# Kernel tuning notes

Hardware: AMD Instinct MI355X
Metric: run time of the kernel (lower is better)

Reference implementation:

```python
import jax, jax.numpy as jnp
import numpy as np

EPS = 1e-5


def _bn(x, g, b, m, v):
    # eval-mode BatchNorm over the last (channel) axis
    return g * (x - m) * jax.lax.rsqrt(v + EPS) + b


def setup_inputs() -> dict:
    key = jax.random.key(0)
    ks = jax.random.split(key, 16)
    B, N, K, C, Cout, G = 2, 16384, 32, 64, 64, 10
    inp = {
        "points": jax.random.normal(ks[0], (B, N, 3), jnp.float32),
        "features": jax.random.normal(ks[1], (B, N, C), jnp.float32),
        "grouped_idx": jax.random.randint(ks[2], (B, N, K), 0, N, jnp.int32),
        # pos_proj: Conv2d(geo_ch, in_ch, 1) + BN + ReLU
        "W_pos": jax.random.normal(ks[3], (C, G), jnp.float32) / np.sqrt(G),
        "b_pos": jnp.zeros((C,), jnp.float32),
        "bn1_g": jnp.ones((C,), jnp.float32),
        "bn1_b": jnp.zeros((C,), jnp.float32),
        "bn1_m": jax.random.normal(ks[4], (C,), jnp.float32) * 0.1,
        "bn1_v": jax.random.uniform(ks[5], (C,), jnp.float32, 0.5, 1.5),
        # gcm_layer: Conv2d(in_ch, in_ch, 1) + BN + ReLU
        "W_gcm": jax.random.normal(ks[6], (C, C), jnp.float32) / np.sqrt(C),
        "b_gcm": jnp.zeros((C,), jnp.float32),
        "bn2_g": jnp.ones((C,), jnp.float32),
        "bn2_b": jnp.zeros((C,), jnp.float32),
        "bn2_m": jax.random.normal(ks[7], (C,), jnp.float32) * 0.1,
        "bn2_v": jax.random.uniform(ks[8], (C,), jnp.float32, 0.5, 1.5),
        # att_conv_catfea: Linear(nsample, 1)
        "W_att": jax.random.normal(ks[9], (K,), jnp.float32) / np.sqrt(K),
        "b_att": jnp.zeros((), jnp.float32),
        # out_layer: Linear(in_ch, out_ch) + LayerNorm + ReLU
        "W_out": jax.random.normal(ks[10], (Cout, C), jnp.float32) / np.sqrt(C),
        "b_out": jnp.zeros((Cout,), jnp.float32),
        "ln_g": jnp.ones((Cout,), jnp.float32),
        "ln_b": jnp.zeros((Cout,), jnp.float32),
    }
    return inp


def reference(points, features, grouped_idx, W_pos, b_pos, bn1_g, bn1_b, bn1_m, bn1_v,
              W_gcm, b_gcm, bn2_g, bn2_b, bn2_m, bn2_v, W_att, b_att,
              W_out, b_out, ln_g, ln_b):
    gather = jax.vmap(lambda arr, idx: arr[idx])  # [N,C],[N,K] -> [N,K,C]
    grouped_points = gather(points, grouped_idx)          # [B,N,K,3]
    grouped_f = gather(features, grouped_idx)             # [B,N,K,C]

    # legacy geometric encoding: [xi, xj, xi - xj, ||xi - xj||] -> geo_ch = 10
    xi = points[:, :, None, :]
    diff = xi - grouped_points
    dist = jnp.linalg.norm(diff, axis=-1, keepdims=True)
    geo = jnp.concatenate(
        [jnp.broadcast_to(xi, grouped_points.shape), grouped_points, diff, dist], axis=-1)

    # pos_proj: 1x1 conv == channel linear, + BN + ReLU
    expanded = jax.nn.relu(_bn(jnp.einsum('bnkg,cg->bnkc', geo, W_pos) + b_pos,
                               bn1_g, bn1_b, bn1_m, bn1_v))

    h = grouped_f + expanded
    # gcm_layer
    h = jax.nn.relu(_bn(jnp.einsum('bnkc,dc->bnkd', h, W_gcm) + b_gcm,
                        bn2_g, bn2_b, bn2_m, bn2_v))

    # attention over neighbor dim K -> score per channel, softmax over channels (dim=2 of [B,N,C,1])
    score = jnp.einsum('bnkc,k->bnc', h, W_att) + b_att   # [B,N,C]
    score = jax.nn.softmax(score, axis=-1)
    h = h * score[:, :, None, :]                          # [B,N,K,C]

    pooled = jnp.max(h, axis=2)                           # maxpooling downsample -> [B,N,C]
    res = pooled + features

    # out_layer: Linear + LayerNorm + ReLU
    y = jnp.einsum('bnc,oc->bno', res, W_out) + b_out
    mu = jnp.mean(y, axis=-1, keepdims=True)
    var = jnp.var(y, axis=-1, keepdims=True)
    y = ln_g * (y - mu) * jax.lax.rsqrt(var + EPS) + ln_b
    return jax.nn.relu(y)
```

## Files before the change

### kernel.cpp

```cpp
#include <hip/hip_runtime.h>
#include <hip/hip_bf16.h>

#define EPSF 1e-5f

typedef __attribute__((ext_vector_type(8))) short bf16x8;
typedef __attribute__((ext_vector_type(4))) float f32x4;
typedef __attribute__((ext_vector_type(2))) unsigned int u32x2;
typedef __attribute__((ext_vector_type(4))) unsigned int u32x4;
typedef __attribute__((ext_vector_type(4))) int i32x4;

constexpr int B_ = 2, N_ = 16384;
constexpr int HSTR = 72;
constexpr int RSTR = 72;
constexpr int PPW  = 8;
constexpr int NW   = 8;
constexpr int PPB  = 64;
constexpr int NWG  = (B_ * N_) / PPB;
constexpr int HALF = NWG / 2;
constexpr size_t PP_BYTES = (size_t)B_ * N_ * 16;

__device__ __forceinline__ short f2bf(float f) {
    __hip_bfloat16 h = __float2bfloat16(f);
    short s; __builtin_memcpy(&s, &h, 2); return s;
}
__device__ __forceinline__ unsigned int pkbf(float a, float b) {
    float2 f2; f2.x = a; f2.y = b;
    __hip_bfloat162 h = __float22bfloat162_rn(f2);
    unsigned int u; __builtin_memcpy(&u, &h, 4); return u;
}

__global__ __launch_bounds__(256) void prep_points(
    const float* __restrict__ pts, float* __restrict__ pp)
{
    const int i = blockIdx.x * 256 + threadIdx.x;
    if (i < B_ * N_) {
        f32x4 o = { pts[3 * i], pts[3 * i + 1], pts[3 * i + 2], 0.f };
        ((f32x4*)pp)[i] = o;
    }
}

template<bool PAD>
__global__ __launch_bounds__(512, 2) void bridgenet13(
    const float* __restrict__ points,
    const float* __restrict__ pp,
    const float* __restrict__ features,
    const int*   __restrict__ gidx,
    const float* __restrict__ Wpos,
    const float* __restrict__ bposv,
    const float* __restrict__ bn1g, const float* __restrict__ bn1b,
    const float* __restrict__ bn1m, const float* __restrict__ bn1v,
    const float* __restrict__ Wgcm,
    const float* __restrict__ bgcm,
    const float* __restrict__ bn2g, const float* __restrict__ bn2b,
    const float* __restrict__ bn2m, const float* __restrict__ bn2v,
    const float* __restrict__ Watt,
    const float* __restrict__ batt,
    const float* __restrict__ Wout,
    const float* __restrict__ bout,
    const float* __restrict__ lng, const float* __restrict__ lnb,
    float* __restrict__ out)
{
    __shared__ __align__(16) short hbuf[NW][32 * HSTR];
    __shared__ __align__(16) short resstage[PPB * RSTR];
    __shared__ __align__(16) short wb2[8 * 64 * 8];
    __shared__ __align__(16) short wb3[8 * 64 * 8];

    const int t    = threadIdx.x;
    const int w    = t >> 6;
    const int l    = t & 63;
    const int l15  = l & 15;
    const int quad = l >> 4;
    const int c4   = l15 * 4;

    const int wg  = blockIdx.x;
    const int blk = ((wg & 7) >> 2) * HALF + ((wg >> 3) << 2) + (wg & 3);

    {
        #pragma unroll
        for (int u = 0; u < 2; ++u) {
            const int s  = w * 2 + u;
            const int nt = (s >> 1) & 3, ks = s & 1;
            const float* src = (s < 8 ? Wgcm : Wout) + (c4 + nt) * 64 + ks * 32 + quad * 8;
            const f32x4 w0 = *(const f32x4*)src;
            const f32x4 w1 = *(const f32x4*)(src + 4);
            bf16x8 f;
            #pragma unroll
            for (int j = 0; j < 4; ++j) {
                f[j]     = f2bf(w0[j]);
                f[j + 4] = f2bf(w1[j]);
            }
            short* dst = (s < 8 ? wb2 : wb3);
            *(bf16x8*)&dst[((s & 7) * 64 + l) * 8] = f;
        }
    }

    bf16x8 bposf[4];
    #pragma unroll
    for (int nt = 0; nt < 4; ++nt) {
        const int c = c4 + nt;
        #pragma unroll
        for (int j = 0; j < 8; ++j) {
            const int g = quad * 8 + j;
            bposf[nt][j] = f2bf(g < 10 ? Wpos[c * 10 + g] : 0.f);
        }
    }
    f32x4 ps1, pb1, ps2, pb2;
    {
        const f32x4 g1 = *(const f32x4*)(bn1g + c4);
        const f32x4 b1 = *(const f32x4*)(bn1b + c4);
        const f32x4 m1 = *(const f32x4*)(bn1m + c4);
        const f32x4 v1 = *(const f32x4*)(bn1v + c4);
        const f32x4 bp = *(const f32x4*)(bposv + c4);
        const f32x4 g2 = *(const f32x4*)(bn2g + c4);
        const f32x4 b2 = *(const f32x4*)(bn2b + c4);
        const f32x4 m2 = *(const f32x4*)(bn2m + c4);
        const f32x4 v2 = *(const f32x4*)(bn2v + c4);
        const f32x4 bg = *(const f32x4*)(bgcm + c4);
        #pragma unroll
        for (int j = 0; j < 4; ++j) {
            ps1[j] = g1[j] * rsqrtf(v1[j] + EPSF);
            pb1[j] = ps1[j] * (bp[j] - m1[j]) + b1[j];
            ps2[j] = g2[j] * rsqrtf(v2[j] + EPSF);
            pb2[j] = ps2[j] * (bg[j] - m2[j]) + b2[j];
        }
    }
    float wat[2][4];
    #pragma unroll
    for (int mt = 0; mt < 2; ++mt)
        #pragma unroll
        for (int r = 0; r < 4; ++r)
            wat[mt][r] = Watt[mt * 16 + quad * 4 + r];
    const float battv = batt[0];

    const f32x4 zero4 = {0.f, 0.f, 0.f, 0.f};
    short* hb = hbuf[w];
    const int base = blk * PPB + w * PPW;
    const int bb   = ((blk * PPB) >> 14) * N_;

    const float* __restrict__ fb  = features + (size_t)bb * 64;
    const float* __restrict__ ppb = pp + (size_t)bb * 4;
    const int*   __restrict__ gb  = gidx + (size_t)base * 32;

    auto LOADI = [&](int i, i32x4 (&gi)[2]) {
        gi[0] = *(const i32x4*)(gb + i * 32 + quad * 4);
        gi[1] = *(const i32x4*)(gb + i * 32 + 16 + quad * 4);
    };
    auto LOADD = [&](int i, const i32x4 (&gi)[2],
                     f32x4 (&f4)[2][4], bf16x8 (&ageo)[2], f32x4& resid) {
        #pragma unroll
        for (int mt = 0; mt < 2; ++mt)
            #pragma unroll
            for (int r = 0; r < 4; ++r)
                f4[mt][r] = *(const f32x4*)(fb + (((unsigned)gi[mt][r]) << 6) + c4);
        const int pt = base + i;
        resid = *(const f32x4*)(features + (size_t)pt * 64 + c4);
        int gv[2];
        gv[0] = gb[i * 32 + l15];
        gv[1] = gb[i * 32 + 16 + l15];
        float xi0, xi1, xi2, px[2], py[2], pz[2];
        if (PAD) {
            const f32x4 x4 = *(const f32x4*)(pp + (size_t)pt * 4);
            xi0 = x4[0]; xi1 = x4[1]; xi2 = x4[2];
            #pragma unroll
            for (int mt = 0; mt < 2; ++mt) {
                const f32x4 p4 = *(const f32x4*)(ppb + (((unsigned)gv[mt]) << 2));
                px[mt] = p4[0]; py[mt] = p4[1]; pz[mt] = p4[2];
            }
        } else {
            xi0 = points[(size_t)pt * 3];
            xi1 = points[(size_t)pt * 3 + 1];
            xi2 = points[(size_t)pt * 3 + 2];
            #pragma unroll
            for (int mt = 0; mt < 2; ++mt) {
                const float* ppt = points + (size_t)(bb + gv[mt]) * 3;
                px[mt] = ppt[0]; py[mt] = ppt[1]; pz[mt] = ppt[2];
            }
        }
        #pragma unroll
        for (int mt = 0; mt < 2; ++mt) {
            const float dx = xi0 - px[mt], dy = xi1 - py[mt], dz = xi2 - pz[mt];
            const float dist = __builtin_amdgcn_sqrtf(dx * dx + dy * dy + dz * dz);
            u32x4 u = {0u, 0u, 0u, 0u};
            if (quad == 0) {
                u[0] = pkbf(xi0, xi1); u[1] = pkbf(xi2, px[mt]);
                u[2] = pkbf(py[mt], pz[mt]); u[3] = pkbf(dx, dy);
            } else if (quad == 1) {
                u[0] = pkbf(dz, dist);
            }
            __builtin_memcpy(&ageo[mt], &u, 16);
        }
    };

    auto COMPUTE = [&](const f32x4 (&f4)[2][4], const bf16x8 (&ageo)[2],
                       const f32x4& resid, int i) {
        __builtin_amdgcn_s_setprio(1);
        f32x4 acc1[2][4];
        #pragma unroll
        for (int mt = 0; mt < 2; ++mt)
            #pragma unroll
            for (int nt = 0; nt < 4; ++nt)
                acc1[mt][nt] = __builtin_amdgcn_mfma_f32_16x16x32_bf16(
                    ageo[mt], bposf[nt], zero4, 0, 0, 0);
        __builtin_amdgcn_s_setprio(0);

        #pragma unroll
        for (int mt = 0; mt < 2; ++mt)
            #pragma unroll
            for (int r = 0; r < 4; ++r) {
                const int k = mt * 16 + quad * 4 + r;
                float v[4];
                #pragma unroll
                for (int j = 0; j < 4; ++j)
                    v[j] = f4[mt][r][j] + fmaxf(ps1[j] * acc1[mt][j][r] + pb1[j], 0.f);
                u32x2 hv = { pkbf(v[0], v[1]), pkbf(v[2], v[3]) };
                *(u32x2*)&hb[k * HSTR + c4] = hv;
            }

        bf16x8 a2[2][2];
        #pragma unroll
        for (int mt = 0; mt < 2; ++mt)
            #pragma unroll
            for (int ks = 0; ks < 2; ++ks)
                a2[mt][ks] = *(const bf16x8*)&hb[(mt * 16 + l15) * HSTR + ks * 32 + quad * 8];
        __builtin_amdgcn_s_setprio(1);
        f32x4 acc2[2][4];
        #pragma unroll
        for (int nt = 0; nt < 4; ++nt) {
            const bf16x8 b0 = *(const bf16x8*)&wb2[((nt * 2 + 0) * 64 + l) * 8];
            const bf16x8 b1 = *(const bf16x8*)&wb2[((nt * 2 + 1) * 64 + l) * 8];
            #pragma unroll
            for (int mt = 0; mt < 2; ++mt) {
                f32x4 a = __builtin_amdgcn_mfma_f32_16x16x32_bf16(a2[mt][0], b0, zero4, 0, 0, 0);
                acc2[mt][nt] = __builtin_amdgcn_mfma_f32_16x16x32_bf16(a2[mt][1], b1, a, 0, 0, 0);
            }
        }
        __builtin_amdgcn_s_setprio(0);

        float res[4];
        {
            float sp[4], mk[4];
            #pragma unroll
            for (int nt = 0; nt < 4; ++nt) {
                sp[nt] = 0.f; mk[nt] = 0.f;
                #pragma unroll
                for (int mt = 0; mt < 2; ++mt)
                    #pragma unroll
                    for (int r = 0; r < 4; ++r) {
                        const float h2 = fmaxf(ps2[nt] * acc2[mt][nt][r] + pb2[nt], 0.f);
                        sp[nt] += h2 * wat[mt][r];
                        mk[nt] = fmaxf(mk[nt], h2);
                    }
                sp[nt] += __shfl_xor(sp[nt], 16);
                sp[nt] += __shfl_xor(sp[nt], 32);
                mk[nt] = fmaxf(mk[nt], __shfl_xor(mk[nt], 16));
                mk[nt] = fmaxf(mk[nt], __shfl_xor(mk[nt], 32));
            }
            float e[4], s = 0.f;
            #pragma unroll
            for (int nt = 0; nt < 4; ++nt) { e[nt] = __expf(sp[nt] + battv); s += e[nt]; }
            #pragma unroll
            for (int o = 1; o < 16; o <<= 1) s += __shfl_xor(s, o);
            const float inv = __builtin_amdgcn_rcpf(s);
            #pragma unroll
            for (int nt = 0; nt < 4; ++nt)
                res[nt] = e[nt] * inv * mk[nt] + resid[nt];
        }
        if (quad == 0) {
            u32x2 rv = { pkbf(res[0], res[1]), pkbf(res[2], res[3]) };
            *(u32x2*)&resstage[(w * PPW + i) * RSTR + c4] = rv;
        }
    };

    i32x4 giA[2], giB[2];
    LOADI(0, giA);
    LOADI(1, giB);
    f32x4  f4A[2][4], f4B[2][4];
    bf16x8 agA[2],   agB[2];
    f32x4  rsA,      rsB;
    LOADD(0, giA, f4A, agA, rsA);

    __syncthreads();

    for (int ip = 0; ip < PPW; ip += 2) {
        LOADD(ip + 1, giB, f4B, agB, rsB);
        if (ip + 2 < PPW) LOADI(ip + 2, giA);
        COMPUTE(f4A, agA, rsA, ip);
        if (ip + 2 < PPW) LOADD(ip + 2, giA, f4A, agA, rsA);
        if (ip + 3 < PPW) LOADI(ip + 3, giB);
        COMPUTE(f4B, agB, rsB, ip + 1);
    }

    __syncthreads();

    {
        const int g = w >> 1;
        const f32x4 lngv  = *(const f32x4*)(lng + c4);
        const f32x4 lnbv  = *(const f32x4*)(lnb + c4);
        const f32x4 boutv = *(const f32x4*)(bout + c4);
        bf16x8 a3[2];
        #pragma unroll
        for (int ks = 0; ks < 2; ++ks)
            a3[ks] = *(const bf16x8*)&resstage[(g * 16 + l15) * RSTR + ks * 32 + quad * 8];
        f32x4 acc3[4];
        #pragma unroll
        for (int nt = 0; nt < 4; ++nt) {
            const bf16x8 b0 = *(const bf16x8*)&wb3[((nt * 2 + 0) * 64 + l) * 8];
            const bf16x8 b1 = *(const bf16x8*)&wb3[((nt * 2 + 1) * 64 + l) * 8];
            f32x4 a = __builtin_amdgcn_mfma_f32_16x16x32_bf16(a3[0], b0, zero4, 0, 0, 0);
            acc3[nt] = __builtin_amdgcn_mfma_f32_16x16x32_bf16(a3[1], b1, a, 0, 0, 0);
        }
        #pragma unroll
        for (int u = 0; u < 2; ++u) {
            const int r = (w & 1) * 2 + u;
            float y[4], s = 0.f;
            #pragma unroll
            for (int nt = 0; nt < 4; ++nt) { y[nt] = acc3[nt][r] + boutv[nt]; s += y[nt]; }
            #pragma unroll
            for (int o = 1; o < 16; o <<= 1) s += __shfl_xor(s, o);
            const float mu = s * (1.f / 64.f);
            float dv[4], v2 = 0.f;
            #pragma unroll
            for (int nt = 0; nt < 4; ++nt) { dv[nt] = y[nt] - mu; v2 += dv[nt] * dv[nt]; }
            #pragma unroll
            for (int o = 1; o < 16; o <<= 1) v2 += __shfl_xor(v2, o);
            const float rs = rsqrtf(v2 * (1.f / 64.f) + EPSF);
            const int pto = blk * PPB + g * 16 + quad * 4 + r;
            f32x4 ov;
            #pragma unroll
            for (int nt = 0; nt < 4; ++nt)
                ov[nt] = fmaxf(lngv[nt] * dv[nt] * rs + lnbv[nt], 0.f);
            *(f32x4*)(out + (size_t)pto * 64 + c4) = ov;
        }
    }
}

extern "C" void kernel_launch(void* const* d_in, const int* in_sizes, int n_in,
                              void* d_out, int out_size, void* d_ws, size_t ws_size,
                              hipStream_t stream) {
    const float* points   = (const float*)d_in[0];
    const float* features = (const float*)d_in[1];
    const int*   gidxp    = (const int*)d_in[2];
    const bool   pad      = (ws_size >= PP_BYTES);
    float* pp = (float*)d_ws;
    if (pad) {
        hipLaunchKernelGGL(prep_points, dim3((B_ * N_ + 255) / 256), dim3(256), 0, stream,
                           points, pp);
        hipLaunchKernelGGL((bridgenet13<true>), dim3(NWG), dim3(512), 0, stream,
            points, pp, features, gidxp,
            (const float*)d_in[3],  (const float*)d_in[4],
            (const float*)d_in[5],  (const float*)d_in[6],  (const float*)d_in[7],  (const float*)d_in[8],
            (const float*)d_in[9],  (const float*)d_in[10],
            (const float*)d_in[11], (const float*)d_in[12], (const float*)d_in[13], (const float*)d_in[14],
            (const float*)d_in[15], (const float*)d_in[16],
            (const float*)d_in[17], (const float*)d_in[18],
            (const float*)d_in[19], (const float*)d_in[20],
            (float*)d_out);
    } else {
        hipLaunchKernelGGL((bridgenet13<false>), dim3(NWG), dim3(512), 0, stream,
            points, pp, features, gidxp,
            (const float*)d_in[3],  (const float*)d_in[4],
            (const float*)d_in[5],  (const float*)d_in[6],  (const float*)d_in[7],  (const float*)d_in[8],
            (const float*)d_in[9],  (const float*)d_in[10],
            (const float*)d_in[11], (const float*)d_in[12], (const float*)d_in[13], (const float*)d_in[14],
            (const float*)d_in[15], (const float*)d_in[16],
            (const float*)d_in[17], (const float*)d_in[18],
            (const float*)d_in[19], (const float*)d_in[20],
            (float*)d_out);
    }
}
```

Before: 157.4 us.

## Halve waves per block and interleave two points per wave with double-buffered LDS

Each block now runs 4 waves instead of 8, and each wave handles 16 points. The per-point compute is split into a FRONT stage (the two MFMA layers) and a BACK stage (attention, softmax, pooling). Two points are processed in parallel into separate LDS buffers, so the MFMA work of one point can hide the other's dependency chains, and gathers for the next pair are issued between stages. The cost is more registers per wave (four in-flight gather sets) and fewer waves per CU for hiding memory latency, with a risk of spills or lower occupancy.

```diff
diff --git a/kernel.cpp b/kernel.cpp
--- a/kernel.cpp
+++ b/kernel.cpp
@@ -12,8 +12,8 @@
 constexpr int B_ = 2, N_ = 16384;
 constexpr int HSTR = 72;
 constexpr int RSTR = 72;
-constexpr int PPW  = 8;
-constexpr int NW   = 8;
+constexpr int PPW  = 16;
+constexpr int NW   = 4;
 constexpr int PPB  = 64;
 constexpr int NWG  = (B_ * N_) / PPB;
 constexpr int HALF = NWG / 2;
@@ -40,7 +40,7 @@
 }
 
 template<bool PAD>
-__global__ __launch_bounds__(512, 2) void bridgenet13(
+__global__ __launch_bounds__(256, 2) void bridgenet14(
     const float* __restrict__ points,
     const float* __restrict__ pp,
     const float* __restrict__ features,
@@ -60,7 +60,7 @@
     const float* __restrict__ lng, const float* __restrict__ lnb,
     float* __restrict__ out)
 {
-    __shared__ __align__(16) short hbuf[NW][32 * HSTR];
+    __shared__ __align__(16) short hbuf[NW][2][32 * HSTR];
     __shared__ __align__(16) short resstage[PPB * RSTR];
     __shared__ __align__(16) short wb2[8 * 64 * 8];
     __shared__ __align__(16) short wb3[8 * 64 * 8];
@@ -77,8 +77,8 @@
 
     {
         #pragma unroll
-        for (int u = 0; u < 2; ++u) {
-            const int s  = w * 2 + u;
+        for (int u = 0; u < 4; ++u) {
+            const int s  = w * 4 + u;
             const int nt = (s >> 1) & 3, ks = s & 1;
             const float* src = (s < 8 ? Wgcm : Wout) + (c4 + nt) * 64 + ks * 32 + quad * 8;
             const f32x4 w0 = *(const f32x4*)src;
@@ -133,7 +133,6 @@
     const float battv = batt[0];
 
     const f32x4 zero4 = {0.f, 0.f, 0.f, 0.f};
-    short* hb = hbuf[w];
     const int base = blk * PPB + w * PPW;
     const int bb   = ((blk * PPB) >> 14) * N_;
 
@@ -191,8 +190,8 @@
         }
     };
 
-    auto COMPUTE = [&](const f32x4 (&f4)[2][4], const bf16x8 (&ageo)[2],
-                       const f32x4& resid, int i) {
+    auto FRONT = [&](short* hb, const f32x4 (&f4)[2][4], const bf16x8 (&ageo)[2],
+                     f32x4 (&acc2)[2][4]) {
         __builtin_amdgcn_s_setprio(1);
         f32x4 acc1[2][4];
         #pragma unroll
@@ -223,7 +222,6 @@
             for (int ks = 0; ks < 2; ++ks)
                 a2[mt][ks] = *(const bf16x8*)&hb[(mt * 16 + l15) * HSTR + ks * 32 + quad * 8];
         __builtin_amdgcn_s_setprio(1);
-        f32x4 acc2[2][4];
         #pragma unroll
         for (int nt = 0; nt < 4; ++nt) {
             const bf16x8 b0 = *(const bf16x8*)&wb2[((nt * 2 + 0) * 64 + l) * 8];
@@ -235,7 +233,9 @@
             }
         }
         __builtin_amdgcn_s_setprio(0);
-
+    };
+
+    auto BACK = [&](int i, const f32x4 (&acc2)[2][4], const f32x4& resid) {
         float res[4];
         {
             float sp[4], mk[4];
@@ -271,36 +271,57 @@
         }
     };
 
-    i32x4 giA[2], giB[2];
-    LOADI(0, giA);
-    LOADI(1, giB);
-    f32x4  f4A[2][4], f4B[2][4];
-    bf16x8 agA[2],   agB[2];
-    f32x4  rsA,      rsB;
-    LOADD(0, giA, f4A, agA, rsA);
+    short* hb0 = &hbuf[w][0][0];
+    short* hb1 = &hbuf[w][1][0];
+
+    i32x4 giA0[2], giA1[2], giB0[2], giB1[2];
+    LOADI(0, giA0); LOADI(1, giA1);
+    LOADI(2, giB0); LOADI(3, giB1);
+    f32x4  f4A0[2][4], f4A1[2][4], f4B0[2][4], f4B1[2][4];
+    bf16x8 agA0[2], agA1[2], agB0[2], agB1[2];
+    f32x4  rsA0, rsA1, rsB0, rsB1;
+    LOADD(0, giA0, f4A0, agA0, rsA0);
+    LOADD(1, giA1, f4A1, agA1, rsA1);
 
     __syncthreads();
 
-    for (int ip = 0; ip < PPW; ip += 2) {
-        LOADD(ip + 1, giB, f4B, agB, rsB);
-        if (ip + 2 < PPW) LOADI(ip + 2, giA);
-        COMPUTE(f4A, agA, rsA, ip);
-        if (ip + 2 < PPW) LOADD(ip + 2, giA, f4A, agA, rsA);
-        if (ip + 3 < PPW) LOADI(ip + 3, giB);
-        COMPUTE(f4B, agB, rsB, ip + 1);
+    #pragma unroll
+    for (int ip = 0; ip < PPW; ip += 4) {
+        f32x4 accA0[2][4], accA1[2][4];
+        FRONT(hb0, f4A0, agA0, accA0);
+        FRONT(hb1, f4A1, agA1, accA1);
+        if (ip + 2 < PPW) {
+            LOADD(ip + 2, giB0, f4B0, agB0, rsB0);
+            LOADD(ip + 3, giB1, f4B1, agB1, rsB1);
+            if (ip + 4 < PPW) { LOADI(ip + 4, giA0); LOADI(ip + 5, giA1); }
+        }
+        BACK(ip, accA0, rsA0);
+        BACK(ip + 1, accA1, rsA1);
+
+        if (ip + 2 < PPW) {
+            f32x4 accB0[2][4], accB1[2][4];
+            FRONT(hb0, f4B0, agB0, accB0);
+            FRONT(hb1, f4B1, agB1, accB1);
+            if (ip + 4 < PPW) {
+                LOADD(ip + 4, giA0, f4A0, agA0, rsA0);
+                LOADD(ip + 5, giA1, f4A1, agA1, rsA1);
+                if (ip + 6 < PPW) { LOADI(ip + 6, giB0); LOADI(ip + 7, giB1); }
+            }
+            BACK(ip + 2, accB0, rsB0);
+            BACK(ip + 3, accB1, rsB1);
+        }
     }
 
     __syncthreads();
 
     {
-        const int g = w >> 1;
         const f32x4 lngv  = *(const f32x4*)(lng + c4);
         const f32x4 lnbv  = *(const f32x4*)(lnb + c4);
         const f32x4 boutv = *(const f32x4*)(bout + c4);
         bf16x8 a3[2];
         #pragma unroll
         for (int ks = 0; ks < 2; ++ks)
-            a3[ks] = *(const bf16x8*)&resstage[(g * 16 + l15) * RSTR + ks * 32 + quad * 8];
+            a3[ks] = *(const bf16x8*)&resstage[(w * 16 + l15) * RSTR + ks * 32 + quad * 8];
         f32x4 acc3[4];
         #pragma unroll
         for (int nt = 0; nt < 4; ++nt) {
@@ -310,11 +331,10 @@
             acc3[nt] = __builtin_amdgcn_mfma_f32_16x16x32_bf16(a3[1], b1, a, 0, 0, 0);
         }
         #pragma unroll
-        for (int u = 0; u < 2; ++u) {
-            const int r = (w & 1) * 2 + u;
+        for (int u = 0; u < 4; ++u) {
             float y[4], s = 0.f;
             #pragma unroll
-            for (int nt = 0; nt < 4; ++nt) { y[nt] = acc3[nt][r] + boutv[nt]; s += y[nt]; }
+            for (int nt = 0; nt < 4; ++nt) { y[nt] = acc3[nt][u] + boutv[nt]; s += y[nt]; }
             #pragma unroll
             for (int o = 1; o < 16; o <<= 1) s += __shfl_xor(s, o);
             const float mu = s * (1.f / 64.f);
@@ -324,7 +344,7 @@
             #pragma unroll
             for (int o = 1; o < 16; o <<= 1) v2 += __shfl_xor(v2, o);
             const float rs = rsqrtf(v2 * (1.f / 64.f) + EPSF);
-            const int pto = blk * PPB + g * 16 + quad * 4 + r;
+            const int pto = blk * PPB + w * 16 + quad * 4 + u;
             f32x4 ov;
             #pragma unroll
             for (int nt = 0; nt < 4; ++nt)
@@ -345,7 +365,7 @@
     if (pad) {
         hipLaunchKernelGGL(prep_points, dim3((B_ * N_ + 255) / 256), dim3(256), 0, stream,
                            points, pp);
-        hipLaunchKernelGGL((bridgenet13<true>), dim3(NWG), dim3(512), 0, stream,
+        hipLaunchKernelGGL((bridgenet14<true>), dim3(NWG), dim3(256), 0, stream,
             points, pp, features, gidxp,
             (const float*)d_in[3],  (const float*)d_in[4],
             (const float*)d_in[5],  (const float*)d_in[6],  (const float*)d_in[7],  (const float*)d_in[8],
@@ -356,7 +376,7 @@
             (const float*)d_in[19], (const float*)d_in[20],
             (float*)d_out);
     } else {
-        hipLaunchKernelGGL((bridgenet13<false>), dim3(NWG), dim3(512), 0, stream,
+        hipLaunchKernelGGL((bridgenet14<false>), dim3(NWG), dim3(256), 0, stream,
             points, pp, features, gidxp,
             (const float*)d_in[3],  (const float*)d_in[4],
             (const float*)d_in[5],  (const float*)d_in[6],  (const float*)d_in[7],  (const float*)d_in[8],
```

After: 152.5 us (median of 3 runs). 1.03x faster.
